# Performance work log

Hardware: AMD Instinct MI355X
Metric: run time of the kernel (lower is better)

The kernel has to match this reference:

```python
import jax, jax.numpy as jnp
import numpy as np

B, N, LATENT, HIDDEN = 65536, 32, 32, 64

def setup_inputs() -> dict:
    key = jax.random.key(0)
    ks = jax.random.split(key, 16)
    def xavier(k, shape):
        fan_in, fan_out = shape[1], shape[0]
        lim = float(np.sqrt(6.0 / (fan_in + fan_out)))
        return jax.random.uniform(k, shape, jnp.float32, -lim, lim)
    inp = {
        'x_sensors': jax.random.normal(ks[0], (B, N), jnp.float32),
        'state_x': jax.random.uniform(ks[1], (B, 1), jnp.float32),
        # GAT: W Linear(1, LATENT, bias=False), a Linear(2*LATENT, 1, bias=False), xavier init
        'W_gat': xavier(ks[2], (LATENT, 1)),
        'a_gat': xavier(ks[3], (1, 2 * LATENT)),
        # pooling: Linear(LATENT, LATENT//2) -> Tanh -> Linear(LATENT//2, 1) -> Softmax(dim=1)
        'p1_w': xavier(ks[4], (LATENT // 2, LATENT)),
        'p1_b': jnp.zeros((LATENT // 2,), jnp.float32),
        'p2_w': xavier(ks[5], (1, LATENT // 2)),
        'p2_b': jnp.zeros((1,), jnp.float32),
        # MNN: MonotonicLinear raw weights uniform(-0.5, 0.5), zero bias
        'm1_w': jax.random.uniform(ks[6], (HIDDEN, 1), jnp.float32, -0.5, 0.5),
        'm1_b': jnp.zeros((HIDDEN,), jnp.float32),
        'm2_w': jax.random.uniform(ks[7], (HIDDEN, HIDDEN), jnp.float32, -0.5, 0.5),
        'm2_b': jnp.zeros((HIDDEN,), jnp.float32),
        'm3_w': jax.random.uniform(ks[8], (LATENT, HIDDEN), jnp.float32, -0.5, 0.5),
        'm3_b': jnp.zeros((LATENT,), jnp.float32),
    }
    return inp

def reference(x_sensors, state_x, W_gat, a_gat, p1_w, p1_b, p2_w, p2_b,
              m1_w, m1_b, m2_w, m2_b, m3_w, m3_b):
    # --- GAT encoder ---
    # h = x_sensors[..., None] (B,N,1); Wh = h @ W_gat.T -> (B,N,D)
    Wh = jnp.einsum('bn,d->bnd', x_sensors, W_gat[:, 0])
    # e_ij = leakyrelu(a^T [Wh_i || Wh_j]) decomposed: a = [a1; a2]
    a1, a2 = a_gat[0, :LATENT], a_gat[0, LATENT:]
    s_i = jnp.einsum('bnd,d->bn', Wh, a1)  # contribution of Wh_i
    s_j = jnp.einsum('bnd,d->bn', Wh, a2)  # contribution of Wh_j
    e = jax.nn.leaky_relu(s_i[:, :, None] + s_j[:, None, :], 0.2)  # (B,N,N)
    alpha = jax.nn.softmax(e, axis=2)  # dropout is identity in eval
    h_prime = jnp.einsum('bij,bjd->bid', alpha, Wh)  # (B,N,D)
    # pooling: softmax over sensor dim (dim=1)
    t = jnp.tanh(h_prime @ p1_w.T + p1_b)
    beta = jax.nn.softmax(t @ p2_w.T + p2_b, axis=1)  # (B,N,1)
    z_enc = jnp.sum(h_prime * beta, axis=1)  # (B,D)
    # --- MNN decoder (exp-positive weights) ---
    h1 = jnp.tanh(state_x @ jnp.exp(m1_w).T + m1_b)
    h2 = jnp.tanh(h1 @ jnp.exp(m2_w).T + m2_b)
    z_dec = h2 @ jnp.exp(m3_w).T + m3_b  # (B,D)
    return (z_enc, z_dec)
```

## Files before the change

kernel.cpp:

```cpp
#include <hip/hip_runtime.h>
#include <hip/hip_bf16.h>

#define LOG2E     1.4426950408889634f
#define TWO_LOG2E 2.8853900817779268f

typedef __attribute__((ext_vector_type(8))) _Float16 f16x8;
typedef __attribute__((ext_vector_type(4))) float    f32x4;
typedef __attribute__((ext_vector_type(2))) float    f32x2;

__device__ __forceinline__ float rcp_(float x){ return __builtin_amdgcn_rcpf(x); }
__device__ __forceinline__ float ex2_(float x){ return __builtin_amdgcn_exp2f(x); }

template<int K>
__device__ __forceinline__ float quadbc(float v){
  constexpr int ctrl = K * 0x55;
  return __int_as_float(__builtin_amdgcn_mov_dpp(__float_as_int(v), ctrl, 0xf, 0xf, true));
}

union FragH { f16x8 v; uint32_t w[4]; uint4 u4; };

__device__ __forceinline__ uint32_t pkh(float a, float b){
  union { _Float16 h; uint16_t u; } ca, cb;
  ca.h = (_Float16)a; cb.h = (_Float16)b;
  return (uint32_t)ca.u | ((uint32_t)cb.u << 16);
}
__device__ __forceinline__ void exph8(const float* __restrict__ src, FragH& out){
  float4 a = *(const float4*)src;
  float4 b = *(const float4*)(src + 4);
  out.w[0] = pkh(__expf(a.x), __expf(a.y));
  out.w[1] = pkh(__expf(a.z), __expf(a.w));
  out.w[2] = pkh(__expf(b.x), __expf(b.y));
  out.w[3] = pkh(__expf(b.z), __expf(b.w));
}

#define WS_FG1   0
#define WS_FG2   2048
#define WS_TBL   3072
#define WS_E1S   3584
#define WS_M1B   3648
#define WS_SCAL  3712

#define TBL_N     512
#define TBL_SCALE 25.6f
#define TBL_LO    -10.0f
#define TBL_CMAX  9.9f

__global__ __launch_bounds__(256) void IDSSM_pre(
    const float* __restrict__ Wg,  const float* __restrict__ ag,
    const float* __restrict__ p1w, const float* __restrict__ p1b,
    const float* __restrict__ p2w, const float* __restrict__ p2b,
    const float* __restrict__ m1w, const float* __restrict__ m1b,
    const float* __restrict__ m2w, const float* __restrict__ m3w,
    float* __restrict__ ws)
{
  const int blk = blockIdx.x;
  const int tid = threadIdx.x;
  const int l  = tid & 63;
  const int bl = l & 15, gt = l >> 4;
  if (blk < 2){
    const int s  = (blk*256 + tid) >> 6;
    const int mt = s >> 1, kt = s & 1;
    FragH h;
    exph8(m2w + (bl + 16*mt)*64 + 8*gt + 32*kt, h);
    *(uint4*)(ws + WS_FG1 + (size_t)(s*64 + l)*4) = h.u4;
  } else if (blk == 2){
    const int s2  = tid >> 6;
    const int mt2 = s2 >> 1, kt2 = s2 & 1;
    FragH h;
    exph8(m3w + (bl + 16*mt2)*64 + 8*gt + 32*kt2, h);
    *(uint4*)(ws + WS_FG2 + (size_t)(s2*64 + l)*4) = h.u4;
  } else if (blk == 3){
    __shared__ float qs[16], pb_[16], pw[16], u0s[1];
    if (tid < 16){
      float acc = 0.f;
      #pragma unroll
      for (int d = 0; d < 32; ++d) acc += p1w[tid*32 + d] * Wg[d];
      qs[tid]  = acc * TWO_LOG2E;
      pb_[tid] = p1b[tid] * TWO_LOG2E;
      pw[tid]  = -2.f * p2w[tid];
    }
    if (tid == 16){
      float sp = 0.f;
      #pragma unroll
      for (int k = 0; k < 16; ++k) sp += p2w[k];
      u0s[0] = sp + p2b[0];
    }
    __syncthreads();
    #pragma unroll
    for (int rep = 0; rep < 2; ++rep){
      const int n = tid + rep*256;
      const float c = TBL_LO + (float)n * (1.0f/TBL_SCALE);
      float u = u0s[0];
      #pragma unroll
      for (int k = 0; k < 16; ++k){
        float E = ex2_(fmaf(c, qs[k], pb_[k]));
        u = fmaf(pw[k], rcp_(E + 1.f), u);
      }
      ws[WS_TBL + n] = u * LOG2E;
    }
  } else {
    if (tid < 64){
      ws[WS_E1S + tid] = __expf(m1w[tid]) * TWO_LOG2E;
      ws[WS_M1B + tid] = m1b[tid] * TWO_LOG2E;
    } else if (tid == 64){
      float A1 = 0.f, A2 = 0.f;
      #pragma unroll
      for (int d = 0; d < 32; ++d){ A1 += Wg[d]*ag[d]; A2 += Wg[d]*ag[32+d]; }
      ws[WS_SCAL + 0] = A1 * LOG2E;
      ws[WS_SCAL + 1] = A2 * LOG2E;
    }
  }
}

#define XJ(J) (((((J)&3))==0) ? xr4[(J)>>2].x : ((((J)&3))==1) ? xr4[(J)>>2].y : \
               ((((J)&3))==2) ? xr4[(J)>>2].z : xr4[(J)>>2].w)

#define ATT_J(JQ, JR) { \
    const float Fj_ = quadbc<JQ>(Fjr[JR]); \
    const float Fq_ = quadbc<JQ>(Fqr[JR]); \
    const float xj_ = XJ(JQ*8+JR); \
    const f32x2 Fj2_ = {Fj_,Fj_}, Fq2_ = {Fq_,Fq_}, xj2_ = {xj_,xj_}; \
    f32x2 pe_; \
    pe_ = __builtin_elementwise_max(Ei2[0]*Fj2_, Eq2[0]*Fq2_); s2[0] = s2[0] + pe_; sx2[0] = sx2[0] + pe_*xj2_; \
    pe_ = __builtin_elementwise_max(Ei2[1]*Fj2_, Eq2[1]*Fq2_); s2[1] = s2[1] + pe_; sx2[1] = sx2[1] + pe_*xj2_; \
    pe_ = __builtin_elementwise_max(Ei2[2]*Fj2_, Eq2[2]*Fq2_); s2[2] = s2[2] + pe_; sx2[2] = sx2[2] + pe_*xj2_; \
    pe_ = __builtin_elementwise_max(Ei2[3]*Fj2_, Eq2[3]*Fq2_); s2[3] = s2[3] + pe_; sx2[3] = sx2[3] + pe_*xj2_; \
  }
#define ATT_Q(JQ) ATT_J(JQ,0) ATT_J(JQ,1) ATT_J(JQ,2) ATT_J(JQ,3) \
                  ATT_J(JQ,4) ATT_J(JQ,5) ATT_J(JQ,6) ATT_J(JQ,7)

__global__ __launch_bounds__(256, 4) void IDSSM_main(
    const float* __restrict__ xs,  const float* __restrict__ stx,
    const float* __restrict__ Wg,  const float* __restrict__ m2b,
    const float* __restrict__ m3b, const float* __restrict__ ws,
    float* __restrict__ out, int B)
{
  __shared__ float tbl[TBL_N];
  const int tid = threadIdx.x;
  const int lb  = tid >> 2;
  const int q   = tid & 3;
  const int b0  = blockIdx.x * 64;
  const int b   = b0 + lb;
  const bool valid = (b < B);
  const int rsrc = valid ? b : (B - 1);

  const float2 tco = *(const float2*)(ws + WS_TBL + tid*2);
  const float A1p = ws[WS_SCAL + 0];
  const float A2p = ws[WS_SCAL + 1];

  const float4* xrow4 = (const float4*)(xs + (size_t)rsrc*32);
  float4 xr4[8];
  #pragma unroll
  for (int t = 0; t < 8; ++t) xr4[t] = xrow4[t];
  float4 xia = xrow4[q*2], xib = xrow4[q*2 + 1];
  float xi[8] = { xia.x, xia.y, xia.z, xia.w, xib.x, xib.y, xib.z, xib.w };

  tbl[tid*2]     = tco.x;
  tbl[tid*2 + 1] = tco.y;

  float Fjr[8], Fqr[8];
  #pragma unroll
  for (int t = 0; t < 8; ++t){
    const float tv = A2p * xi[t];
    Fjr[t] = ex2_(tv);
    Fqr[t] = ex2_(0.2f * tv);
  }
  f32x2 Ei2[4], Eq2[4], s2[4], sx2[4];
  #pragma unroll
  for (int p = 0; p < 4; ++p){
    const float sa = A1p * xi[2*p], sb = A1p * xi[2*p + 1];
    Ei2[p] = (f32x2){ ex2_(sa), ex2_(sb) };
    Eq2[p] = (f32x2){ ex2_(0.2f*sa), ex2_(0.2f*sb) };
    s2[p]  = (f32x2)(0.f);
    sx2[p] = (f32x2)(0.f);
  }
  ATT_Q(0) ATT_Q(1) ATT_Q(2) ATT_Q(3)

  __syncthreads();

  float Zs = 0.f, Zd = 0.f;
  #pragma unroll
  for (int p = 0; p < 4; ++p){
    #pragma unroll
    for (int h = 0; h < 2; ++h){
      const float sv  = h ? s2[p].y  : s2[p].x;
      const float sxv = h ? sx2[p].y : sx2[p].x;
      const float c  = sxv * rcp_(sv);
      const float cc = fminf(fmaxf(c, TBL_LO), TBL_CMAX);
      const float f  = (cc - TBL_LO) * TBL_SCALE;
      const int   n  = (int)f;
      const float fr = f - (float)n;
      const float t0 = tbl[n];
      const float t1 = tbl[n + 1];
      const float eb = ex2_(fmaf(fr, t1 - t0, t0));
      Zs = fmaf(eb, c, Zs);
      Zd += eb;
    }
  }
  Zs += __shfl_xor(Zs, 1);  Zd += __shfl_xor(Zd, 1);
  Zs += __shfl_xor(Zs, 2);  Zd += __shfl_xor(Zd, 2);
  const float Z = Zs * rcp_(Zd);

  if (valid){
    const float4 w0 = ((const float4*)Wg)[q*2 + 0];
    const float4 w1 = ((const float4*)Wg)[q*2 + 1];
    float4* o = (float4*)(out + (size_t)b*32 + q*8);
    o[0] = make_float4(Z*w0.x, Z*w0.y, Z*w0.z, Z*w0.w);
    o[1] = make_float4(Z*w1.x, Z*w1.y, Z*w1.z, Z*w1.w);
  }

  const int lane = tid & 63;
  const int wv   = tid >> 6;
  const int gt   = lane >> 4;
  const int bl   = lane & 15;
  const int bd   = b0 + wv*16 + bl;
  const float sx0 = stx[(bd < B) ? bd : (B-1)];

  uint4 fg1r[8];
  #pragma unroll
  for (int s = 0; s < 8; ++s)
    fg1r[s] = *(const uint4*)(ws + WS_FG1 + (size_t)(s*64 + lane)*4);

  FragH h1f[2];
  #pragma unroll
  for (int kt = 0; kt < 2; ++kt){
    const int g0 = 8*gt + 32*kt;
    const float4* e1p = (const float4*)(ws + WS_E1S + g0);
    const float4* m1p = (const float4*)(ws + WS_M1B + g0);
    float4 ea = e1p[0], eb4 = e1p[1];
    float4 ma = m1p[0], mb4 = m1p[1];
    float ev[8] = { ea.x,ea.y,ea.z,ea.w, eb4.x,eb4.y,eb4.z,eb4.w };
    float mv[8] = { ma.x,ma.y,ma.z,ma.w, mb4.x,mb4.y,mb4.z,mb4.w };
    float hv[8];
    #pragma unroll
    for (int j = 0; j < 8; ++j){
      float E = ex2_(fmaf(sx0, ev[j], mv[j]));
      hv[j] = fmaf(-2.f, rcp_(E + 1.f), 1.f);
    }
    #pragma unroll
    for (int jw = 0; jw < 4; ++jw)
      h1f[kt].w[jw] = pkh(hv[2*jw], hv[2*jw+1]);
  }

  f32x4 acc[4];
  #pragma unroll
  for (int mt = 0; mt < 4; ++mt){
    float4 bi = *(const float4*)(m2b + 16*mt + 4*gt);
    acc[mt][0]=bi.x; acc[mt][1]=bi.y; acc[mt][2]=bi.z; acc[mt][3]=bi.w;
  }
  #pragma unroll
  for (int mt = 0; mt < 4; ++mt){
    #pragma unroll
    for (int kt = 0; kt < 2; ++kt){
      FragH A; A.u4 = fg1r[mt*2 + kt];
      acc[mt] = __builtin_amdgcn_mfma_f32_16x16x32_f16(A.v, h1f[kt].v, acc[mt], 0, 0, 0);
    }
  }

  uint4 fg2r[4];
  #pragma unroll
  for (int s = 0; s < 4; ++s)
    fg2r[s] = *(const uint4*)(ws + WS_FG2 + (size_t)(s*64 + lane)*4);

  uint32_t Wp[4][2];
  #pragma unroll
  for (int mt = 0; mt < 4; ++mt){
    float t0 = fmaf(-2.f, rcp_(ex2_(acc[mt][0]*TWO_LOG2E) + 1.f), 1.f);
    float t1 = fmaf(-2.f, rcp_(ex2_(acc[mt][1]*TWO_LOG2E) + 1.f), 1.f);
    float t2 = fmaf(-2.f, rcp_(ex2_(acc[mt][2]*TWO_LOG2E) + 1.f), 1.f);
    float t3 = fmaf(-2.f, rcp_(ex2_(acc[mt][3]*TWO_LOG2E) + 1.f), 1.f);
    Wp[mt][0] = pkh(t0, t1);
    Wp[mt][1] = pkh(t2, t3);
  }

  FragH B2[2];
  const int hiSel = gt >> 1;
  #pragma unroll
  for (int kt2 = 0; kt2 < 2; ++kt2){
    #pragma unroll
    for (int jw = 0; jw < 4; ++jw){
      const int sl = bl + 16*(((jw>>1) + 2*gt) & 3);
      const int w  = jw & 1;
      uint32_t c0 = (uint32_t)__shfl((int)Wp[2*kt2+0][w], sl);
      uint32_t c1 = (uint32_t)__shfl((int)Wp[2*kt2+1][w], sl);
      B2[kt2].w[jw] = hiSel ? c1 : c0;
    }
  }

  f32x4 acc2[2];
  #pragma unroll
  for (int mt2 = 0; mt2 < 2; ++mt2){
    float4 bi = *(const float4*)(m3b + 16*mt2 + 4*gt);
    acc2[mt2][0]=bi.x; acc2[mt2][1]=bi.y; acc2[mt2][2]=bi.z; acc2[mt2][3]=bi.w;
  }
  #pragma unroll
  for (int mt2 = 0; mt2 < 2; ++mt2){
    #pragma unroll
    for (int kt2 = 0; kt2 < 2; ++kt2){
      FragH A; A.u4 = fg2r[mt2*2 + kt2];
      acc2[mt2] = __builtin_amdgcn_mfma_f32_16x16x32_f16(A.v, B2[kt2].v, acc2[mt2], 0, 0, 0);
    }
  }

  if (bd < B){
    float* o = out + (size_t)B*32 + (size_t)bd*32;
    *(float4*)(o + 4*gt)      = make_float4(acc2[0][0], acc2[0][1], acc2[0][2], acc2[0][3]);
    *(float4*)(o + 16 + 4*gt) = make_float4(acc2[1][0], acc2[1][1], acc2[1][2], acc2[1][3]);
  }
}

extern "C" void kernel_launch(void* const* d_in, const int* in_sizes, int n_in,
                              void* d_out, int out_size, void* d_ws, size_t ws_size,
                              hipStream_t stream)
{
  const float* xs  = (const float*)d_in[0];
  const float* stx = (const float*)d_in[1];
  const float* Wg  = (const float*)d_in[2];
  const float* ag  = (const float*)d_in[3];
  const float* p1w = (const float*)d_in[4];
  const float* p1b = (const float*)d_in[5];
  const float* p2w = (const float*)d_in[6];
  const float* p2b = (const float*)d_in[7];
  const float* m1w = (const float*)d_in[8];
  const float* m1b = (const float*)d_in[9];
  const float* m2w = (const float*)d_in[10];
  const float* m2b = (const float*)d_in[11];
  const float* m3w = (const float*)d_in[12];
  const float* m3b = (const float*)d_in[13];
  float* out = (float*)d_out;
  float* ws  = (float*)d_ws;
  const int B = in_sizes[0] / 32;

  hipLaunchKernelGGL(IDSSM_pre, dim3(5), dim3(256), 0, stream,
                     Wg, ag, p1w, p1b, p2w, p2b, m1w, m1b, m2w, m3w, ws);
  const int nblk = (B + 63) / 64;
  hipLaunchKernelGGL(IDSSM_main, dim3(nblk), dim3(256), 0, stream,
                     xs, stx, Wg, m2b, m3b, ws, out, B);
}
```

Measured before the change: 24.54 us.

## Fuse weight preprocessing into main kernel and drop separate pre-launch

Removes the separate preprocessing kernel and has every block recompute the exp'd MFMA weight fragments into shared memory, along with the pooling lookup table and the attention scalars. The table shrinks from 512 to 256 entries so one pass of threads fills it. The goal is to eliminate a kernel launch and the workspace round trip. In exchange, each of the 1024 blocks redundantly does exp work, adds 12KB of LDS that may cut occupancy, and the coarser table may reduce accuracy.

Measured after the change: 24.27 us. No clear change (-1.1%).

```diff
diff --git a/kernel.cpp b/kernel.cpp
--- a/kernel.cpp
+++ b/kernel.cpp
@@ -33,84 +33,10 @@
   out.w[3] = pkh(__expf(b.z), __expf(b.w));
 }
 
-#define WS_FG1   0
-#define WS_FG2   2048
-#define WS_TBL   3072
-#define WS_E1S   3584
-#define WS_M1B   3648
-#define WS_SCAL  3712
-
-#define TBL_N     512
-#define TBL_SCALE 25.6f
+#define TBL_N     256
+#define TBL_SCALE 12.8f
 #define TBL_LO    -10.0f
 #define TBL_CMAX  9.9f
-
-__global__ __launch_bounds__(256) void IDSSM_pre(
-    const float* __restrict__ Wg,  const float* __restrict__ ag,
-    const float* __restrict__ p1w, const float* __restrict__ p1b,
-    const float* __restrict__ p2w, const float* __restrict__ p2b,
-    const float* __restrict__ m1w, const float* __restrict__ m1b,
-    const float* __restrict__ m2w, const float* __restrict__ m3w,
-    float* __restrict__ ws)
-{
-  const int blk = blockIdx.x;
-  const int tid = threadIdx.x;
-  const int l  = tid & 63;
-  const int bl = l & 15, gt = l >> 4;
-  if (blk < 2){
-    const int s  = (blk*256 + tid) >> 6;
-    const int mt = s >> 1, kt = s & 1;
-    FragH h;
-    exph8(m2w + (bl + 16*mt)*64 + 8*gt + 32*kt, h);
-    *(uint4*)(ws + WS_FG1 + (size_t)(s*64 + l)*4) = h.u4;
-  } else if (blk == 2){
-    const int s2  = tid >> 6;
-    const int mt2 = s2 >> 1, kt2 = s2 & 1;
-    FragH h;
-    exph8(m3w + (bl + 16*mt2)*64 + 8*gt + 32*kt2, h);
-    *(uint4*)(ws + WS_FG2 + (size_t)(s2*64 + l)*4) = h.u4;
-  } else if (blk == 3){
-    __shared__ float qs[16], pb_[16], pw[16], u0s[1];
-    if (tid < 16){
-      float acc = 0.f;
-      #pragma unroll
-      for (int d = 0; d < 32; ++d) acc += p1w[tid*32 + d] * Wg[d];
-      qs[tid]  = acc * TWO_LOG2E;
-      pb_[tid] = p1b[tid] * TWO_LOG2E;
-      pw[tid]  = -2.f * p2w[tid];
-    }
-    if (tid == 16){
-      float sp = 0.f;
-      #pragma unroll
-      for (int k = 0; k < 16; ++k) sp += p2w[k];
-      u0s[0] = sp + p2b[0];
-    }
-    __syncthreads();
-    #pragma unroll
-    for (int rep = 0; rep < 2; ++rep){
-      const int n = tid + rep*256;
-      const float c = TBL_LO + (float)n * (1.0f/TBL_SCALE);
-      float u = u0s[0];
-      #pragma unroll
-      for (int k = 0; k < 16; ++k){
-        float E = ex2_(fmaf(c, qs[k], pb_[k]));
-        u = fmaf(pw[k], rcp_(E + 1.f), u);
-      }
-      ws[WS_TBL + n] = u * LOG2E;
-    }
-  } else {
-    if (tid < 64){
-      ws[WS_E1S + tid] = __expf(m1w[tid]) * TWO_LOG2E;
-      ws[WS_M1B + tid] = m1b[tid] * TWO_LOG2E;
-    } else if (tid == 64){
-      float A1 = 0.f, A2 = 0.f;
-      #pragma unroll
-      for (int d = 0; d < 32; ++d){ A1 += Wg[d]*ag[d]; A2 += Wg[d]*ag[32+d]; }
-      ws[WS_SCAL + 0] = A1 * LOG2E;
-      ws[WS_SCAL + 1] = A2 * LOG2E;
-    }
-  }
-}
 
 #define XJ(J) (((((J)&3))==0) ? xr4[(J)>>2].x : ((((J)&3))==1) ? xr4[(J)>>2].y : \
                ((((J)&3))==2) ? xr4[(J)>>2].z : xr4[(J)>>2].w)
@@ -131,11 +57,18 @@
 
 __global__ __launch_bounds__(256, 4) void IDSSM_main(
     const float* __restrict__ xs,  const float* __restrict__ stx,
-    const float* __restrict__ Wg,  const float* __restrict__ m2b,
-    const float* __restrict__ m3b, const float* __restrict__ ws,
+    const float* __restrict__ Wg,  const float* __restrict__ ag,
+    const float* __restrict__ p1w, const float* __restrict__ p1b,
+    const float* __restrict__ p2w, const float* __restrict__ p2b,
+    const float* __restrict__ m1w, const float* __restrict__ m1b,
+    const float* __restrict__ m2w, const float* __restrict__ m2b,
+    const float* __restrict__ m3w, const float* __restrict__ m3b,
     float* __restrict__ out, int B)
 {
+  __shared__ uint4 fgl[768];
   __shared__ float tbl[TBL_N];
+  __shared__ float qsh[16], pbb[16], p2wn[16], scal[3];
+
   const int tid = threadIdx.x;
   const int lb  = tid >> 2;
   const int q   = tid & 3;
@@ -144,10 +77,6 @@
   const bool valid = (b < B);
   const int rsrc = valid ? b : (B - 1);
 
-  const float2 tco = *(const float2*)(ws + WS_TBL + tid*2);
-  const float A1p = ws[WS_SCAL + 0];
-  const float A2p = ws[WS_SCAL + 1];
-
   const float4* xrow4 = (const float4*)(xs + (size_t)rsrc*32);
   float4 xr4[8];
   #pragma unroll
@@ -155,9 +84,57 @@
   float4 xia = xrow4[q*2], xib = xrow4[q*2 + 1];
   float xi[8] = { xia.x, xia.y, xia.z, xia.w, xib.x, xib.y, xib.z, xib.w };
 
-  tbl[tid*2]     = tco.x;
-  tbl[tid*2 + 1] = tco.y;
-
+  #pragma unroll
+  for (int rep = 0; rep < 3; ++rep){
+    const int s    = tid + rep*256;
+    const int slot = s >> 6;
+    const int l    = s & 63;
+    const int bl_  = l & 15;
+    const int gt_  = l >> 4;
+    const float* src;
+    if (slot < 8) src = m2w + (bl_ + 16*(slot>>1))*64 + 8*gt_ + 32*(slot&1);
+    else { const int s2 = slot - 8;
+           src = m3w + (bl_ + 16*(s2>>1))*64 + 8*gt_ + 32*(s2&1); }
+    FragH h;
+    exph8(src, h);
+    fgl[slot*64 + l] = h.u4;
+  }
+  if (tid >= 64 && tid < 80){
+    const int k = tid - 64;
+    float acc = 0.f;
+    #pragma unroll
+    for (int d = 0; d < 32; ++d) acc += p1w[k*32 + d] * Wg[d];
+    qsh[k]  = acc * TWO_LOG2E;
+    pbb[k]  = p1b[k] * TWO_LOG2E;
+    p2wn[k] = -2.f * p2w[k];
+  }
+  if (tid == 80){
+    float A1 = 0.f, A2 = 0.f;
+    #pragma unroll
+    for (int d = 0; d < 32; ++d){ A1 += Wg[d]*ag[d]; A2 += Wg[d]*ag[32+d]; }
+    scal[0] = A1 * LOG2E;
+    scal[1] = A2 * LOG2E;
+  }
+  if (tid == 81){
+    float sp = 0.f;
+    #pragma unroll
+    for (int k = 0; k < 16; ++k) sp += p2w[k];
+    scal[2] = sp + p2b[0];
+  }
+  __syncthreads();
+
+  {
+    const float c = TBL_LO + (float)tid * (1.0f/TBL_SCALE);
+    float u = scal[2];
+    #pragma unroll
+    for (int k = 0; k < 16; ++k){
+      float E = ex2_(fmaf(c, qsh[k], pbb[k]));
+      u = fmaf(p2wn[k], rcp_(E + 1.f), u);
+    }
+    tbl[tid] = u * LOG2E;
+  }
+
+  const float A1p = scal[0], A2p = scal[1];
   float Fjr[8], Fqr[8];
   #pragma unroll
   for (int t = 0; t < 8; ++t){
@@ -216,25 +193,21 @@
   const int bd   = b0 + wv*16 + bl;
   const float sx0 = stx[(bd < B) ? bd : (B-1)];
 
-  uint4 fg1r[8];
-  #pragma unroll
-  for (int s = 0; s < 8; ++s)
-    fg1r[s] = *(const uint4*)(ws + WS_FG1 + (size_t)(s*64 + lane)*4);
-
   FragH h1f[2];
   #pragma unroll
   for (int kt = 0; kt < 2; ++kt){
     const int g0 = 8*gt + 32*kt;
-    const float4* e1p = (const float4*)(ws + WS_E1S + g0);
-    const float4* m1p = (const float4*)(ws + WS_M1B + g0);
-    float4 ea = e1p[0], eb4 = e1p[1];
-    float4 ma = m1p[0], mb4 = m1p[1];
-    float ev[8] = { ea.x,ea.y,ea.z,ea.w, eb4.x,eb4.y,eb4.z,eb4.w };
-    float mv[8] = { ma.x,ma.y,ma.z,ma.w, mb4.x,mb4.y,mb4.z,mb4.w };
+    const float4* w1p = (const float4*)(m1w + g0);
+    const float4* b1p = (const float4*)(m1b + g0);
+    float4 wa = w1p[0], wb = w1p[1];
+    float4 ba = b1p[0], bb = b1p[1];
+    float wv8[8] = { wa.x,wa.y,wa.z,wa.w, wb.x,wb.y,wb.z,wb.w };
+    float bv8[8] = { ba.x,ba.y,ba.z,ba.w, bb.x,bb.y,bb.z,bb.w };
     float hv[8];
     #pragma unroll
     for (int j = 0; j < 8; ++j){
-      float E = ex2_(fmaf(sx0, ev[j], mv[j]));
+      const float e1 = ex2_(wv8[j] * LOG2E) * TWO_LOG2E;
+      const float E  = ex2_(fmaf(sx0, e1, bv8[j] * TWO_LOG2E));
       hv[j] = fmaf(-2.f, rcp_(E + 1.f), 1.f);
     }
     #pragma unroll
@@ -252,15 +225,10 @@
   for (int mt = 0; mt < 4; ++mt){
     #pragma unroll
     for (int kt = 0; kt < 2; ++kt){
-      FragH A; A.u4 = fg1r[mt*2 + kt];
+      FragH A; A.u4 = fgl[(mt*2 + kt)*64 + lane];
       acc[mt] = __builtin_amdgcn_mfma_f32_16x16x32_f16(A.v, h1f[kt].v, acc[mt], 0, 0, 0);
     }
   }
-
-  uint4 fg2r[4];
-  #pragma unroll
-  for (int s = 0; s < 4; ++s)
-    fg2r[s] = *(const uint4*)(ws + WS_FG2 + (size_t)(s*64 + lane)*4);
 
   uint32_t Wp[4][2];
   #pragma unroll
@@ -297,7 +265,7 @@
   for (int mt2 = 0; mt2 < 2; ++mt2){
     #pragma unroll
     for (int kt2 = 0; kt2 < 2; ++kt2){
-      FragH A; A.u4 = fg2r[mt2*2 + kt2];
+      FragH A; A.u4 = fgl[512 + (mt2*2 + kt2)*64 + lane];
       acc2[mt2] = __builtin_amdgcn_mfma_f32_16x16x32_f16(A.v, B2[kt2].v, acc2[mt2], 0, 0, 0);
     }
   }
@@ -328,12 +296,9 @@
   const float* m3w = (const float*)d_in[12];
   const float* m3b = (const float*)d_in[13];
   float* out = (float*)d_out;
-  float* ws  = (float*)d_ws;
   const int B = in_sizes[0] / 32;
-
-  hipLaunchKernelGGL(IDSSM_pre, dim3(5), dim3(256), 0, stream,
-                     Wg, ag, p1w, p1b, p2w, p2b, m1w, m1b, m2w, m3w, ws);
   const int nblk = (B + 63) / 64;
   hipLaunchKernelGGL(IDSSM_main, dim3(nblk), dim3(256), 0, stream,
-                     xs, stx, Wg, m2b, m3b, ws, out, B);
-}
+                     xs, stx, Wg, ag, p1w, p1b, p2w, p2b,
+                     m1w, m1b, m2w, m2b, m3w, m3b, out, B);
+}
```
